# Kernel tuning notes

Hardware: AMD Instinct MI355X
Metric: run time of the kernel (lower is better)

## Reference

```python
import jax, jax.numpy as jnp
import numpy as np

B, T, D = 2, 2048, 2048
NH, NKV = 16, 4
HD = D // NH  # 128
BASE, TSL = 10000.0, 1024


def rotary_tables(T, hd, base=BASE, tsl=TSL):
    # Matches Rotary.forward with rd == hd (rd=0 in __init__ -> full head dim).
    ar = jnp.arange(0, hd, 2, dtype=jnp.float32) / hd
    if T <= tsl:
        inv = 1.0 / (base ** ar)
    else:
        # NTK-style rescale; note right-assoc exponent in original torch code:
        # 1/(base * (T/tsl) ** ((rd/(rd-2)) ** ar))
        inv = 1.0 / (base * jnp.power(T / tsl, jnp.power(hd / (hd - 2.0), ar)))
    f = jnp.outer(jnp.arange(T, dtype=jnp.float32), inv)  # [T, hd//2]
    cos = jnp.cos(f)[None, :, None, :]  # [1,T,1,hd//2]
    sin = jnp.sin(f)[None, :, None, :]
    return cos, sin


def apply_rope(x, cos, sin):
    # full-dim rope: split halves, rotate
    h = x.shape[-1] // 2
    x1, x2 = x[..., :h], x[..., h:]
    return jnp.concatenate((x1 * cos + x2 * sin, -x1 * sin + x2 * cos), axis=-1)


def rms_norm(x):
    eps = jnp.finfo(x.dtype).eps
    return x * jax.lax.rsqrt(jnp.mean(x * x, axis=-1, keepdims=True) + eps)


def setup_inputs() -> dict:
    key = jax.random.key(0)
    k0, k1, k2, k3, k4 = jax.random.split(key, 5)
    s = 0.02
    return {
        "x": jax.random.normal(k0, (B, T, D), jnp.float32),
        "qw": jax.random.normal(k1, (NH * HD, D), jnp.float32) * s,
        "kw": jax.random.normal(k2, (NKV * HD, D), jnp.float32) * s,
        "vw": jax.random.normal(k3, (NKV * HD, D), jnp.float32) * s,
        "ow": jax.random.normal(k4, (D, D), jnp.float32) * s,
        "qg": jnp.ones((NH,), jnp.float32),
    }


def reference(x, qw, kw, vw, ow, qg):
    Bx, Tx, Dx = x.shape
    q = (x @ qw.T).reshape(Bx, Tx, NH, HD)
    k = (x @ kw.T).reshape(Bx, Tx, NKV, HD)
    v = (x @ vw.T).reshape(Bx, Tx, NKV, HD)
    q = rms_norm(q)
    k = rms_norm(k)
    cos, sin = rotary_tables(Tx, HD)
    q = apply_rope(q, cos, sin) * qg[None, None, :, None]
    k = apply_rope(k, cos, sin)
    # GQA: repeat kv heads
    r = NH // NKV
    k = jnp.repeat(k, r, axis=2)  # [B,T,NH,HD]
    v = jnp.repeat(v, r, axis=2)
    scale = 1.0 / jnp.sqrt(jnp.asarray(HD, q.dtype))
    scores = jnp.einsum("bqhd,bkhd->bhqk", q, k) * scale  # [B,NH,T,T]
    causal = jnp.tril(jnp.ones((Tx, Tx), dtype=bool))
    scores = jnp.where(causal[None, None, :, :], scores, jnp.asarray(-jnp.inf, scores.dtype))
    attn = jax.nn.softmax(scores, axis=-1)
    y = jnp.einsum("bhqk,bkhd->bqhd", attn, v)  # [B,T,NH,HD]
    return y.reshape(Bx, Tx, Dx) @ ow.T
```

## Files before the change

kernel.cpp:

```cpp
#include <hip/hip_runtime.h>
#include <hip/hip_bf16.h>
#include <stdint.h>


typedef __attribute__((ext_vector_type(8))) short short8;
typedef __attribute__((ext_vector_type(4))) float f32x4;

#define GLOAD16(gp, lp) \
  __builtin_amdgcn_global_load_lds((const __attribute__((address_space(1))) void*)(gp), \
                                   (__attribute__((address_space(3))) void*)(lp), 16, 0, 0)

#define BAR() do { asm volatile("" ::: "memory"); __builtin_amdgcn_s_barrier(); asm volatile("" ::: "memory"); } while (0)

__device__ __forceinline__ float bf2f(unsigned short u) {
  union { unsigned int i; float f; } v; v.i = ((unsigned int)u) << 16; return v.f;
}
__device__ __forceinline__ unsigned short f2bf(float f) {
  union { float fl; unsigned int i; } v; v.fl = f;
  unsigned int r = v.i + 0x7fffu + ((v.i >> 16) & 1u);
  return (unsigned short)(r >> 16);
}

__global__ __launch_bounds__(256) void prep_kernel(
    const float* __restrict__ x, const float* __restrict__ qw,
    const float* __restrict__ kw, const float* __restrict__ vw,
    const float* __restrict__ ow,
    unsigned short* __restrict__ xb, unsigned short* __restrict__ wqkv,
    unsigned short* __restrict__ owb, float* __restrict__ cost, float* __restrict__ sint) {
  const int NX = 2097152;
  const int NW = 1572864;
  const int NO = 1048576;
  const int NT = 131072;
  int tid = blockIdx.x * 256 + threadIdx.x;
  if (tid < NX) {
    float4 v = ((const float4*)x)[tid];
    uint2 o; o.x = (unsigned)f2bf(v.x) | ((unsigned)f2bf(v.y) << 16);
    o.y = (unsigned)f2bf(v.z) | ((unsigned)f2bf(v.w) << 16);
    ((uint2*)xb)[tid] = o;
  } else if (tid < NX + NW) {
    int i = tid - NX; int e = i * 4;
    const float* src = (e < 4194304) ? (qw + e)
                     : (e < 5242880) ? (kw + (e - 4194304))
                                     : (vw + (e - 5242880));
    float4 v = *(const float4*)src;
    uint2 o; o.x = (unsigned)f2bf(v.x) | ((unsigned)f2bf(v.y) << 16);
    o.y = (unsigned)f2bf(v.z) | ((unsigned)f2bf(v.w) << 16);
    ((uint2*)wqkv)[i] = o;
  } else if (tid < NX + NW + NO) {
    int i = tid - NX - NW;
    float4 v = ((const float4*)ow)[i];
    uint2 o; o.x = (unsigned)f2bf(v.x) | ((unsigned)f2bf(v.y) << 16);
    o.y = (unsigned)f2bf(v.z) | ((unsigned)f2bf(v.w) << 16);
    ((uint2*)owb)[i] = o;
  } else if (tid < NX + NW + NO + NT) {
    int i = tid - NX - NW - NO;
    int t = i >> 6, j = i & 63;
    float e = exp2f(0.02272008f * (float)j * (1.0f / 64.0f));
    float inv = 1.0f / (10000.0f * exp2f(e));
    float f = (float)t * inv;
    cost[i] = cosf(f);
    sint[i] = sinf(f);
  }
}

template <int IM, int OUTF>
__global__ __launch_bounds__(512) void gemm8ph(const unsigned short* __restrict__ A,
                                               const unsigned short* __restrict__ Bw,
                                               void* __restrict__ Cp,
                                               int MT, int NTn, int N, int K) {
  extern __shared__ char smc[];
  constexpr int S = IM * 8;
  constexpr int IQ = IM / 2;
  constexpr int ASZ = IM * 2048;
  constexpr int DB = 2 * ASZ + 32768;
  constexpr int AL = (IM * 128) / 512;
  const int tid = threadIdx.x;
  const int l = tid & 63, w = tid >> 6;
  const int lane_r = l & 15, lane_g = l >> 4;
  const int wr = w >> 2, wc = w & 3;

  int qch = (MT * NTn) >> 3;
  int orig = blockIdx.x;
  int wgid = (orig & 7) * qch + (orig >> 3);
  int by = wgid / NTn, bx = wgid - by * NTn;
  const int m0 = by * IM * 32, n0 = bx * 256;

  f32x4 acc[IM][4];
#pragma unroll
  for (int i = 0; i < IM; ++i)
#pragma unroll
    for (int j = 0; j < 4; ++j) acc[i][j] = {0.f, 0.f, 0.f, 0.f};

  const unsigned short* srcA[AL]; int ldA[AL];
#pragma unroll
  for (int t = 0; t < AL; ++t) {
    int idx = t * 512 + tid;
    int rc = idx >> 3, kc = idx & 7;
    int wrp = rc >= S ? 1 : 0, rr = rc & (S - 1);
    int row = wrp * 2 * S + rr;
    srcA[t] = A + (size_t)(m0 + row) * K + (kc ^ (rc & 7)) * 8;
    ldA[t] = idx * 16;
  }
  const unsigned short* srcB[2]; int ldB[2];
#pragma unroll
  for (int t = 0; t < 2; ++t) {
    int idx = t * 512 + tid;
    int rc = idx >> 3, kc = idx & 7;
    int nrow = (rc >> 5) * 64 + (rc & 31);
    srcB[t] = Bw + (size_t)(n0 + nrow) * K + (kc ^ (rc & 7)) * 8;
    ldB[t] = idx * 16;
  }
  const int SK = S * K, JK = 32 * K;

  auto STA = [&](int kt, int ih, int dqb) {
    char* d = smc + dqb + ih * ASZ;
#pragma unroll
    for (int t = 0; t < AL; ++t) GLOAD16(srcA[t] + kt + ih * SK, d + ldA[t]);
  };
  auto STB = [&](int kt, int jh, int dqb) {
    char* d = smc + dqb + 2 * ASZ + jh * 16384;
#pragma unroll
    for (int t = 0; t < 2; ++t) GLOAD16(srcB[t] + kt + jh * JK, d + ldB[t]);
  };

  int oA[IQ][2], oB[2][2];
#pragma unroll
  for (int iq = 0; iq < IQ; ++iq)
#pragma unroll
    for (int ks = 0; ks < 2; ++ks) {
      int rc = wr * S + iq * 16 + lane_r;
      oA[iq][ks] = rc * 128 + ((ks * 64 + lane_g * 16) ^ ((rc & 7) << 4));
    }
#pragma unroll
  for (int jj = 0; jj < 2; ++jj)
#pragma unroll
    for (int ks = 0; ks < 2; ++ks) {
      int rc = wc * 32 + jj * 16 + lane_r;
      oB[jj][ks] = rc * 128 + ((ks * 64 + lane_g * 16) ^ ((rc & 7) << 4));
    }

#define VMC() do { if constexpr (IM == 8) asm volatile("s_waitcnt vmcnt(6)" ::: "memory"); \
                   else                   asm volatile("s_waitcnt vmcnt(5)" ::: "memory"); } while (0)
#define VM0() asm volatile("s_waitcnt vmcnt(0)" ::: "memory")
#define MM(IH, JH, BR) do { \
    __builtin_amdgcn_s_setprio(1); \
    _Pragma("unroll") \
    for (int iq = 0; iq < IQ; ++iq) \
      _Pragma("unroll") \
      for (int jj = 0; jj < 2; ++jj) \
        _Pragma("unroll") \
        for (int ks = 0; ks < 2; ++ks) \
          acc[(IH) * IQ + iq][(JH) * 2 + jj] = __builtin_amdgcn_mfma_f32_16x16x32_bf16( \
              af[iq][ks], BR[jj][ks], acc[(IH) * IQ + iq][(JH) * 2 + jj], 0, 0, 0); \
    __builtin_amdgcn_s_setprio(0); } while (0)

  const int NS = K >> 6;
  STA(0, 0, 0); STB(0, 0, 0); STB(0, 1, 0); STA(0, 1, 0);
  STA(64, 0, DB); STB(64, 0, DB); STB(64, 1, DB);
  VMC();
  BAR();

#pragma unroll 1
  for (int s = 0; s < NS; ++s) {
    const int dq = (s & 1) * DB, dn = DB - dq;
    const char* Ab = smc + dq;
    const char* Bb = Ab + 2 * ASZ;
    short8 af[IQ][2], b0[2][2], b1[2][2];
    if (s + 1 < NS) STA((s + 1) << 6, 1, dn);
#pragma unroll
    for (int iq = 0; iq < IQ; ++iq)
#pragma unroll
      for (int ks = 0; ks < 2; ++ks) af[iq][ks] = *(const short8*)(Ab + oA[iq][ks]);
#pragma unroll
    for (int jj = 0; jj < 2; ++jj)
#pragma unroll
      for (int ks = 0; ks < 2; ++ks) b0[jj][ks] = *(const short8*)(Bb + oB[jj][ks]);
    MM(0, 0, b0);
    BAR();
    if (s + 2 < NS) STA((s + 2) << 6, 0, dq);
#pragma unroll
    for (int jj = 0; jj < 2; ++jj)
#pragma unroll
      for (int ks = 0; ks < 2; ++ks) b1[jj][ks] = *(const short8*)(Bb + 16384 + oB[jj][ks]);
    MM(0, 1, b1);
    BAR();
    if (s + 2 < NS) STB((s + 2) << 6, 0, dq);
#pragma unroll
    for (int iq = 0; iq < IQ; ++iq)
#pragma unroll
      for (int ks = 0; ks < 2; ++ks) af[iq][ks] = *(const short8*)(Ab + ASZ + oA[iq][ks]);
    MM(1, 0, b0);
    BAR();
    if (s + 2 < NS) STB((s + 2) << 6, 1, dq);
    MM(1, 1, b1);
    if (s + 2 < NS) VMC(); else VM0();
    BAR();
  }
#undef VMC
#undef VM0
#undef MM

#pragma unroll
  for (int ih = 0; ih < 2; ++ih)
#pragma unroll
    for (int iq = 0; iq < IQ; ++iq) {
      int row = m0 + wr * 2 * S + ih * S + iq * 16 + lane_g * 4;
#pragma unroll
      for (int j = 0; j < 4; ++j) {
        int col = n0 + wc * 64 + j * 16 + lane_r;
#pragma unroll
        for (int r = 0; r < 4; ++r) {
          float v = acc[ih * IQ + iq][j][r];
          if (OUTF)
            ((float*)Cp)[(size_t)(row + r) * N + col] = v;
          else
            ((unsigned short*)Cp)[(size_t)(row + r) * N + col] = f2bf(v);
        }
      }
    }
}

__global__ __launch_bounds__(256) void normrope_kernel(unsigned short* __restrict__ qkv,
                                                       const float* __restrict__ cost,
                                                       const float* __restrict__ sint,
                                                       const float* __restrict__ qg) {
  const int tid = threadIdx.x, l = tid & 63, w = tid >> 6;
  int row = blockIdx.x * 4 + w;
  int tok = row / 20, hh = row - tok * 20;
  int t = tok & 2047;
  bool isq = hh < 16;
  int col0 = isq ? hh * 128 : 2048 + (hh - 16) * 128;
  unsigned short* p = qkv + (size_t)tok * 3072 + col0 + 2 * l;
  unsigned int u = *(const unsigned int*)p;
  float x0 = bf2f((unsigned short)(u & 0xffffu));
  float x1 = bf2f((unsigned short)(u >> 16));
  float ss = x0 * x0 + x1 * x1;
#pragma unroll
  for (int m = 1; m < 64; m <<= 1) ss += __shfl_xor(ss, m);
  float rn = rsqrtf(ss * (1.0f / 128.0f) + 1.1920928955078125e-07f);
  float n0 = x0 * rn, n1 = x1 * rn;
  float p0 = __shfl_xor(n0, 32);
  float p1 = __shfl_xor(n1, 32);
  int jj = (2 * l) & 63;
  float c0 = cost[t * 64 + jj], c1 = cost[t * 64 + jj + 1];
  float s0 = sint[t * 64 + jj], s1 = sint[t * 64 + jj + 1];
  float o0, o1;
  if (l < 32) { o0 = n0 * c0 + p0 * s0; o1 = n1 * c1 + p1 * s1; }
  else        { o0 = -p0 * s0 + n0 * c0; o1 = -p1 * s1 + n1 * c1; }
  if (isq) { float g = qg[hh] * 0.08838834764831845f; o0 *= g; o1 *= g; }
  *(unsigned int*)p = (unsigned)f2bf(o0) | ((unsigned)f2bf(o1) << 16);
}

__global__ __launch_bounds__(256) void vtrans_kernel(const unsigned short* __restrict__ qkv,
                                                     unsigned short* __restrict__ vtg) {
  __shared__ unsigned short tile[64][132];
  int bid = blockIdx.x;
  int pan = bid & 7, tt = bid >> 3;
  int b = pan >> 2, kvh = pan & 3;
  int t0 = tt * 64;
  const unsigned short* src = qkv + ((size_t)(b * 2048 + t0)) * 3072 + 2560 + kvh * 128;
#pragma unroll
  for (int i = 0; i < 8; ++i) {
    int idx = i * 256 + threadIdx.x;
    int row = idx >> 5, c4 = idx & 31;
    uint2 v = *(const uint2*)(src + (size_t)row * 3072 + c4 * 4);
    *(uint2*)&tile[row][c4 * 4] = v;
  }
  __syncthreads();
  unsigned short* dst = vtg + (size_t)pan * 262144 + t0;
#pragma unroll
  for (int i = 0; i < 8; ++i) {
    int idx = i * 256 + threadIdx.x;
    int d = idx >> 4, tc = idx & 15;
    unsigned short a0 = tile[tc * 4 + 0][d], a1 = tile[tc * 4 + 1][d];
    unsigned short a2 = tile[tc * 4 + 2][d], a3 = tile[tc * 4 + 3][d];
    uint2 o; o.x = (unsigned)a0 | ((unsigned)a1 << 16);
    o.y = (unsigned)a2 | ((unsigned)a3 << 16);
    *(uint2*)(dst + (size_t)d * 2048 + tc * 4) = o;
  }
}

__global__ __launch_bounds__(512) void attn_fa4(const unsigned short* __restrict__ qkv,
                                                const unsigned short* __restrict__ vtg,
                                                unsigned short* __restrict__ y) {
  extern __shared__ char smc[];
  const int tid = threadIdx.x;
  const int l = tid & 63, w = tid >> 6;
  const int lane_r = l & 15, lane_g = l >> 4;

  int n = blockIdx.x;
  int pan = n & 7;
  int b = pan >> 2, kvh = pan & 3;
  int idx2 = n >> 3;
  int h = kvh * 4 + (idx2 & 3);
  int pairIdx = idx2 >> 2;
  const size_t rowbase = (size_t)b * 2048;
  const unsigned short* kvK = qkv + rowbase * 3072;
  const unsigned short* vtp = vtg + (size_t)pan * 262144;

  int kg[2], vg[2], sl[2];
#pragma unroll
  for (int t = 0; t < 2; ++t) {
    int idx = t * 512 + tid;
    { int row = idx >> 4, c = idx & 15, gc = c ^ (row & 7);
      kg[t] = row * 3072 + 2048 + kvh * 128 + gc * 8; }
    { int d = idx >> 3, c = idx & 7, gc = c ^ (d & 7);
      vg[t] = d * 2048 + gc * 8; }
    sl[t] = idx * 16;
  }
  const int swz = (lane_r & 7) << 4;
  int oK[4][4];
#pragma unroll
  for (int ct = 0; ct < 4; ++ct)
#pragma unroll
    for (int ks = 0; ks < 4; ++ks)
      oK[ct][ks] = ((ct * 16 + lane_r) * 256 + ks * 64 + lane_g * 16) ^ swz;
  int oV[2][8];
#pragma unroll
  for (int kk = 0; kk < 2; ++kk)
#pragma unroll
    for (int dt = 0; dt < 8; ++dt)
      oV[kk][dt] = ((dt * 16 + lane_r) * 128 + kk * 64 + lane_g * 16) ^ swz;
  const int pbase = 65536 + w * 2048;
  int pw_off[4];
#pragma unroll
  for (int ct = 0; ct < 4; ++ct)
    pw_off[ct] = pbase + lane_r * 128 + ((ct * 32 + lane_g * 8) ^ swz);
  int pr_off[2];
#pragma unroll
  for (int kk = 0; kk < 2; ++kk)
    pr_off[kk] = pbase + lane_r * 128 + ((kk * 64 + lane_g * 16) ^ swz);

  auto STAGE = [&](int tile, int bufsel) {
    const unsigned short* srcK = kvK + (size_t)tile * 64 * 3072;
    const unsigned short* srcV = vtp + tile * 64;
    char* kd = smc + bufsel * 16384;
    char* vd = smc + 32768 + bufsel * 16384;
#pragma unroll
    for (int t = 0; t < 2; ++t) {
      GLOAD16(srcK + kg[t], kd + sl[t]);
      GLOAD16(srcV + vg[t], vd + sl[t]);
    }
  };

#pragma unroll 1
  for (int phase = 0; phase < 2; ++phase) {
    const int qt = phase ? pairIdx : 15 - pairIdx;
    const int q0 = qt * 128;
    const int nkb = 2 * qt + 2;
    const int wrow0 = q0 + w * 16;
    const int qrow = wrow0 + lane_r;

    STAGE(0, 0);
    short8 qf[4];
#pragma unroll
    for (int ks = 0; ks < 4; ++ks)
      qf[ks] = *(const short8*)(qkv + (rowbase + qrow) * 3072 + h * 128 + ks * 32 + lane_g * 8);

    f32x4 acc[8];
#pragma unroll
    for (int dt = 0; dt < 8; ++dt) acc[dt] = {0.f, 0.f, 0.f, 0.f};
    float mrun = -1e30f, lrun = 0.f;

    __syncthreads();

#pragma unroll 1
    for (int kb = 0; kb < nkb; ++kb) {
      const int cur = kb & 1;
      if (kb + 1 < nkb) STAGE(kb + 1, cur ^ 1);
      const int j0 = kb * 64;
      const bool active = (j0 <= wrow0 + 15);
      if (active) {
        const int kbb = cur * 16384;
        f32x4 s[4];
#pragma unroll
        for (int ct = 0; ct < 4; ++ct) s[ct] = {0.f, 0.f, 0.f, 0.f};
        __builtin_amdgcn_s_setprio(1);
#pragma unroll
        for (int ct = 0; ct < 4; ++ct)
#pragma unroll
          for (int ks = 0; ks < 4; ++ks) {
            short8 kf = *(const short8*)(smc + kbb + oK[ct][ks]);
            s[ct] = __builtin_amdgcn_mfma_f32_16x16x32_bf16(kf, qf[ks], s[ct], 0, 0, 0);
          }
        __builtin_amdgcn_s_setprio(0);
        if (j0 + 63 > wrow0) {
#pragma unroll
          for (int ct = 0; ct < 4; ++ct) {
            int kg0 = j0 + ct * 16 + lane_g * 4;
#pragma unroll
            for (int r = 0; r < 4; ++r)
              if (kg0 + r > qrow) s[ct][r] = -1e30f;
          }
        }
        float mx = s[0][0];
#pragma unroll
        for (int ct = 0; ct < 4; ++ct)
#pragma unroll
          for (int r = 0; r < 4; ++r) mx = fmaxf(mx, s[ct][r]);
        mx = fmaxf(mx, __shfl_xor(mx, 16));
        mx = fmaxf(mx, __shfl_xor(mx, 32));
        float mn = fmaxf(mrun, mx);
        float corr = __expf(mrun - mn);
        mrun = mn;
        float rs = 0.f;
#pragma unroll
        for (int ct = 0; ct < 4; ++ct)
#pragma unroll
          for (int r = 0; r < 4; ++r) {
            float e = __expf(s[ct][r] - mn);
            s[ct][r] = e; rs += e;
          }
        rs += __shfl_xor(rs, 16);
        rs += __shfl_xor(rs, 32);
        lrun = lrun * corr + rs;
#pragma unroll
        for (int ct = 0; ct < 4; ++ct) {
          uint2 pv;
          pv.x = (unsigned)f2bf(s[ct][0]) | ((unsigned)f2bf(s[ct][1]) << 16);
          pv.y = (unsigned)f2bf(s[ct][2]) | ((unsigned)f2bf(s[ct][3]) << 16);
          *(uint2*)(smc + pw_off[ct]) = pv;
        }
#pragma unroll
        for (int dt = 0; dt < 8; ++dt)
#pragma unroll
          for (int r = 0; r < 4; ++r) acc[dt][r] *= corr;
        short8 pf[2];
        pf[0] = *(const short8*)(smc + pr_off[0]);
        pf[1] = *(const short8*)(smc + pr_off[1]);
        const int vbase = 32768 + cur * 16384;
        __builtin_amdgcn_s_setprio(1);
#pragma unroll
        for (int kk = 0; kk < 2; ++kk)
#pragma unroll
          for (int dt = 0; dt < 8; ++dt) {
            short8 vf = *(const short8*)(smc + vbase + oV[kk][dt]);
            acc[dt] = __builtin_amdgcn_mfma_f32_16x16x32_bf16(vf, pf[kk], acc[dt], 0, 0, 0);
          }
        __builtin_amdgcn_s_setprio(0);
      }
      __syncthreads();
    }
    float linv = 1.0f / lrun;
    unsigned short* yrow = y + (rowbase + qrow) * 2048 + h * 128;
#pragma unroll
    for (int dt = 0; dt < 8; ++dt) {
      uint2 o;
      o.x = (unsigned)f2bf(acc[dt][0] * linv) | ((unsigned)f2bf(acc[dt][1] * linv) << 16);
      o.y = (unsigned)f2bf(acc[dt][2] * linv) | ((unsigned)f2bf(acc[dt][3] * linv) << 16);
      *(uint2*)(yrow + dt * 16 + lane_g * 4) = o;
    }
  }
}

extern "C" void kernel_launch(void* const* d_in, const int* in_sizes, int n_in,
                              void* d_out, int out_size, void* d_ws, size_t ws_size,
                              hipStream_t stream) {
  (void)in_sizes; (void)n_in; (void)out_size; (void)ws_size;
  const float* x  = (const float*)d_in[0];
  const float* qw = (const float*)d_in[1];
  const float* kw = (const float*)d_in[2];
  const float* vw = (const float*)d_in[3];
  const float* ow = (const float*)d_in[4];
  const float* qg = (const float*)d_in[5];

  char* ws = (char*)d_ws;
  unsigned short* xb   = (unsigned short*)(ws + 0);
  unsigned short* vtg  = (unsigned short*)(ws + 0);
  unsigned short* wqkv = (unsigned short*)(ws + 16777216);
  unsigned short* owb  = (unsigned short*)(ws + 29360128);
  unsigned short* qkvb = (unsigned short*)(ws + 37748736);
  unsigned short* y    = (unsigned short*)(ws + 62914560);
  float* cost          = (float*)(ws + 79691776);
  float* sint          = (float*)(ws + 80216064);

  prep_kernel<<<18944, 256, 0, stream>>>(x, qw, kw, vw, ow, xb, wqkv, owb, cost, sint);
  gemm8ph<8, 0><<<192, 512, 131072, stream>>>(xb, wqkv, qkvb, 16, 12, 3072, 2048);
  normrope_kernel<<<20480, 256, 0, stream>>>(qkvb, cost, sint, qg);
  vtrans_kernel<<<256, 256, 0, stream>>>(qkvb, vtg);
  attn_fa4<<<256, 512, 81920, stream>>>(qkvb, vtg, y);
  gemm8ph<4, 1><<<256, 512, 98304, stream>>>(y, owb, d_out, 32, 8, 2048, 2048);
}
```

Baseline: 200.4 us.

## Rewrite attention with 32x32 MFMA tiles, exp2 softmax and lazy rescaling

The attention kernel now runs 4 waves of 32 query rows each and uses 32x32x16 bf16 MFMAs instead of 16x16x32, which cuts LDS fragment loads and shuffle reductions per score tile. The log2(e) factor is folded into the q scale during norm/rope, so the softmax can use exp2 directly. Rescaling of the running max and accumulator is skipped unless the new max exceeds the old by more than a threshold. Each thread now carries larger accumulators, which raises register pressure, and the skipped rescale lets unnormalised values grow within a bounded range.

```diff
diff --git a/kernel.cpp b/kernel.cpp
--- a/kernel.cpp
+++ b/kernel.cpp
@@ -5,6 +5,7 @@
 
 typedef __attribute__((ext_vector_type(8))) short short8;
 typedef __attribute__((ext_vector_type(4))) float f32x4;
+typedef __attribute__((ext_vector_type(16))) float f32x16;
 
 #define GLOAD16(gp, lp) \
   __builtin_amdgcn_global_load_lds((const __attribute__((address_space(1))) void*)(gp), \
@@ -19,6 +20,9 @@
   union { float fl; unsigned int i; } v; v.fl = f;
   unsigned int r = v.i + 0x7fffu + ((v.i >> 16) & 1u);
   return (unsigned short)(r >> 16);
+}
+__device__ __forceinline__ unsigned pk2(float a, float b) {
+  return (unsigned)f2bf(a) | ((unsigned)f2bf(b) << 16);
 }
 
 __global__ __launch_bounds__(256) void prep_kernel(
@@ -34,8 +38,7 @@
   int tid = blockIdx.x * 256 + threadIdx.x;
   if (tid < NX) {
     float4 v = ((const float4*)x)[tid];
-    uint2 o; o.x = (unsigned)f2bf(v.x) | ((unsigned)f2bf(v.y) << 16);
-    o.y = (unsigned)f2bf(v.z) | ((unsigned)f2bf(v.w) << 16);
+    uint2 o; o.x = pk2(v.x, v.y); o.y = pk2(v.z, v.w);
     ((uint2*)xb)[tid] = o;
   } else if (tid < NX + NW) {
     int i = tid - NX; int e = i * 4;
@@ -43,14 +46,12 @@
                      : (e < 5242880) ? (kw + (e - 4194304))
                                      : (vw + (e - 5242880));
     float4 v = *(const float4*)src;
-    uint2 o; o.x = (unsigned)f2bf(v.x) | ((unsigned)f2bf(v.y) << 16);
-    o.y = (unsigned)f2bf(v.z) | ((unsigned)f2bf(v.w) << 16);
+    uint2 o; o.x = pk2(v.x, v.y); o.y = pk2(v.z, v.w);
     ((uint2*)wqkv)[i] = o;
   } else if (tid < NX + NW + NO) {
     int i = tid - NX - NW;
     float4 v = ((const float4*)ow)[i];
-    uint2 o; o.x = (unsigned)f2bf(v.x) | ((unsigned)f2bf(v.y) << 16);
-    o.y = (unsigned)f2bf(v.z) | ((unsigned)f2bf(v.w) << 16);
+    uint2 o; o.x = pk2(v.x, v.y); o.y = pk2(v.z, v.w);
     ((uint2*)owb)[i] = o;
   } else if (tid < NX + NW + NO + NT) {
     int i = tid - NX - NW - NO;
@@ -247,8 +248,8 @@
   float o0, o1;
   if (l < 32) { o0 = n0 * c0 + p0 * s0; o1 = n1 * c1 + p1 * s1; }
   else        { o0 = -p0 * s0 + n0 * c0; o1 = -p1 * s1 + n1 * c1; }
-  if (isq) { float g = qg[hh] * 0.08838834764831845f; o0 *= g; o1 *= g; }
-  *(unsigned int*)p = (unsigned)f2bf(o0) | ((unsigned)f2bf(o1) << 16);
+  if (isq) { float g = qg[hh] * 0.08838834764831845f * 1.4426950408889634f; o0 *= g; o1 *= g; }
+  *(unsigned int*)p = pk2(o0, o1);
 }
 
 __global__ __launch_bounds__(256) void vtrans_kernel(const unsigned short* __restrict__ qkv,
@@ -280,13 +281,13 @@
   }
 }
 
-__global__ __launch_bounds__(512) void attn_fa4(const unsigned short* __restrict__ qkv,
-                                                const unsigned short* __restrict__ vtg,
-                                                unsigned short* __restrict__ y) {
+__global__ __launch_bounds__(256, 2) void attn_fa5(const unsigned short* __restrict__ qkv,
+                                                   const unsigned short* __restrict__ vtg,
+                                                   unsigned short* __restrict__ y) {
   extern __shared__ char smc[];
   const int tid = threadIdx.x;
   const int l = tid & 63, w = tid >> 6;
-  const int lane_r = l & 15, lane_g = l >> 4;
+  const int lq = l & 31, hi = l >> 5;
 
   int n = blockIdx.x;
   int pan = n & 7;
@@ -298,38 +299,29 @@
   const unsigned short* kvK = qkv + rowbase * 3072;
   const unsigned short* vtp = vtg + (size_t)pan * 262144;
 
-  int kg[2], vg[2], sl[2];
-#pragma unroll
-  for (int t = 0; t < 2; ++t) {
-    int idx = t * 512 + tid;
+  int kg[4], vg[4], sl[4];
+#pragma unroll
+  for (int t = 0; t < 4; ++t) {
+    int idx = t * 256 + tid;
     { int row = idx >> 4, c = idx & 15, gc = c ^ (row & 7);
       kg[t] = row * 3072 + 2048 + kvh * 128 + gc * 8; }
     { int d = idx >> 3, c = idx & 7, gc = c ^ (d & 7);
       vg[t] = d * 2048 + gc * 8; }
     sl[t] = idx * 16;
   }
-  const int swz = (lane_r & 7) << 4;
-  int oK[4][4];
-#pragma unroll
-  for (int ct = 0; ct < 4; ++ct)
-#pragma unroll
-    for (int ks = 0; ks < 4; ++ks)
-      oK[ct][ks] = ((ct * 16 + lane_r) * 256 + ks * 64 + lane_g * 16) ^ swz;
-  int oV[2][8];
-#pragma unroll
-  for (int kk = 0; kk < 2; ++kk)
-#pragma unroll
-    for (int dt = 0; dt < 8; ++dt)
-      oV[kk][dt] = ((dt * 16 + lane_r) * 128 + kk * 64 + lane_g * 16) ^ swz;
-  const int pbase = 65536 + w * 2048;
-  int pw_off[4];
-#pragma unroll
-  for (int ct = 0; ct < 4; ++ct)
-    pw_off[ct] = pbase + lane_r * 128 + ((ct * 32 + lane_g * 8) ^ swz);
-  int pr_off[2];
-#pragma unroll
-  for (int kk = 0; kk < 2; ++kk)
-    pr_off[kk] = pbase + lane_r * 128 + ((kk * 64 + lane_g * 16) ^ swz);
+  const int swq = (lq & 7) << 4;
+  int oxd[8];
+#pragma unroll
+  for (int ds = 0; ds < 8; ++ds) oxd[ds] = (ds * 32 + hi * 16) ^ swq;
+  const int krow = lq * 256;
+  const int vrow = lq * 128;
+  const int pbase = 65536 + w * 4096;
+  const int prow = pbase + lq * 128;
+  int opw[2][4];
+#pragma unroll
+  for (int t = 0; t < 2; ++t)
+#pragma unroll
+    for (int m = 0; m < 4; ++m) opw[t][m] = prow + ((t * 64 + m * 16 + hi * 8) ^ swq);
 
   auto STAGE = [&](int tile, int bufsel) {
     const unsigned short* srcK = kvK + (size_t)tile * 64 * 3072;
@@ -337,7 +329,7 @@
     char* kd = smc + bufsel * 16384;
     char* vd = smc + 32768 + bufsel * 16384;
 #pragma unroll
-    for (int t = 0; t < 2; ++t) {
+    for (int t = 0; t < 4; ++t) {
       GLOAD16(srcK + kg[t], kd + sl[t]);
       GLOAD16(srcV + vg[t], vd + sl[t]);
     }
@@ -348,18 +340,20 @@
     const int qt = phase ? pairIdx : 15 - pairIdx;
     const int q0 = qt * 128;
     const int nkb = 2 * qt + 2;
-    const int wrow0 = q0 + w * 16;
-    const int qrow = wrow0 + lane_r;
+    const int wrow0 = q0 + w * 32;
+    const int qrow = wrow0 + lq;
 
     STAGE(0, 0);
-    short8 qf[4];
-#pragma unroll
-    for (int ks = 0; ks < 4; ++ks)
-      qf[ks] = *(const short8*)(qkv + (rowbase + qrow) * 3072 + h * 128 + ks * 32 + lane_g * 8);
-
-    f32x4 acc[8];
-#pragma unroll
-    for (int dt = 0; dt < 8; ++dt) acc[dt] = {0.f, 0.f, 0.f, 0.f};
+    short8 qf[8];
+#pragma unroll
+    for (int ds = 0; ds < 8; ++ds)
+      qf[ds] = *(const short8*)(qkv + (rowbase + qrow) * 3072 + h * 128 + ds * 16 + hi * 8);
+
+    f32x16 acc[4];
+#pragma unroll
+    for (int dt = 0; dt < 4; ++dt)
+#pragma unroll
+      for (int jj = 0; jj < 16; ++jj) acc[dt][jj] = 0.f;
     float mrun = -1e30f, lrun = 0.f;
 
     __syncthreads();
@@ -369,73 +363,74 @@
       const int cur = kb & 1;
       if (kb + 1 < nkb) STAGE(kb + 1, cur ^ 1);
       const int j0 = kb * 64;
-      const bool active = (j0 <= wrow0 + 15);
-      if (active) {
+      if (j0 <= wrow0 + 31) {
         const int kbb = cur * 16384;
-        f32x4 s[4];
-#pragma unroll
-        for (int ct = 0; ct < 4; ++ct) s[ct] = {0.f, 0.f, 0.f, 0.f};
+        const int vbb = 32768 + cur * 16384;
+        f32x16 s0, s1;
+#pragma unroll
+        for (int jj = 0; jj < 16; ++jj) { s0[jj] = 0.f; s1[jj] = 0.f; }
         __builtin_amdgcn_s_setprio(1);
 #pragma unroll
-        for (int ct = 0; ct < 4; ++ct)
-#pragma unroll
-          for (int ks = 0; ks < 4; ++ks) {
-            short8 kf = *(const short8*)(smc + kbb + oK[ct][ks]);
-            s[ct] = __builtin_amdgcn_mfma_f32_16x16x32_bf16(kf, qf[ks], s[ct], 0, 0, 0);
+        for (int ds = 0; ds < 8; ++ds) {
+          short8 kf = *(const short8*)(smc + kbb + krow + oxd[ds]);
+          s0 = __builtin_amdgcn_mfma_f32_32x32x16_bf16(kf, qf[ds], s0, 0, 0, 0);
+        }
+#pragma unroll
+        for (int ds = 0; ds < 8; ++ds) {
+          short8 kf = *(const short8*)(smc + kbb + 8192 + krow + oxd[ds]);
+          s1 = __builtin_amdgcn_mfma_f32_32x32x16_bf16(kf, qf[ds], s1, 0, 0, 0);
+        }
+        __builtin_amdgcn_s_setprio(0);
+        const int rq = qrow - j0;
+        if (j0 + 63 > wrow0) {
+#pragma unroll
+          for (int jj = 0; jj < 16; ++jj) {
+            int kl = (jj & 3) + 8 * (jj >> 2) + 4 * hi;
+            s0[jj] = (kl > rq) ? -1e30f : s0[jj];
+            s1[jj] = (kl + 32 > rq) ? -1e30f : s1[jj];
           }
-        __builtin_amdgcn_s_setprio(0);
-        if (j0 + 63 > wrow0) {
-#pragma unroll
-          for (int ct = 0; ct < 4; ++ct) {
-            int kg0 = j0 + ct * 16 + lane_g * 4;
-#pragma unroll
-            for (int r = 0; r < 4; ++r)
-              if (kg0 + r > qrow) s[ct][r] = -1e30f;
-          }
-        }
-        float mx = s[0][0];
-#pragma unroll
-        for (int ct = 0; ct < 4; ++ct)
-#pragma unroll
-          for (int r = 0; r < 4; ++r) mx = fmaxf(mx, s[ct][r]);
-        mx = fmaxf(mx, __shfl_xor(mx, 16));
-        mx = fmaxf(mx, __shfl_xor(mx, 32));
-        float mn = fmaxf(mrun, mx);
-        float corr = __expf(mrun - mn);
-        mrun = mn;
+        }
+        float pmax = s0[0];
+#pragma unroll
+        for (int jj = 0; jj < 16; ++jj) pmax = fmaxf(pmax, fmaxf(s0[jj], s1[jj]));
+        pmax = fmaxf(pmax, __shfl_xor(pmax, 32));
+        if (!__all(pmax - mrun <= 11.5f)) {
+          float mn = fmaxf(mrun, pmax);
+          float corr = exp2f(mrun - mn);
+          lrun *= corr;
+#pragma unroll
+          for (int dt = 0; dt < 4; ++dt)
+#pragma unroll
+            for (int jj = 0; jj < 16; ++jj) acc[dt][jj] *= corr;
+          mrun = mn;
+        }
         float rs = 0.f;
 #pragma unroll
-        for (int ct = 0; ct < 4; ++ct)
-#pragma unroll
-          for (int r = 0; r < 4; ++r) {
-            float e = __expf(s[ct][r] - mn);
-            s[ct][r] = e; rs += e;
-          }
-        rs += __shfl_xor(rs, 16);
+        for (int jj = 0; jj < 16; ++jj) {
+          s0[jj] = exp2f(s0[jj] - mrun); rs += s0[jj];
+          s1[jj] = exp2f(s1[jj] - mrun); rs += s1[jj];
+        }
         rs += __shfl_xor(rs, 32);
-        lrun = lrun * corr + rs;
-#pragma unroll
-        for (int ct = 0; ct < 4; ++ct) {
-          uint2 pv;
-          pv.x = (unsigned)f2bf(s[ct][0]) | ((unsigned)f2bf(s[ct][1]) << 16);
-          pv.y = (unsigned)f2bf(s[ct][2]) | ((unsigned)f2bf(s[ct][3]) << 16);
-          *(uint2*)(smc + pw_off[ct]) = pv;
-        }
-#pragma unroll
-        for (int dt = 0; dt < 8; ++dt)
-#pragma unroll
-          for (int r = 0; r < 4; ++r) acc[dt][r] *= corr;
-        short8 pf[2];
-        pf[0] = *(const short8*)(smc + pr_off[0]);
-        pf[1] = *(const short8*)(smc + pr_off[1]);
-        const int vbase = 32768 + cur * 16384;
+        lrun += rs;
+#pragma unroll
+        for (int m = 0; m < 4; ++m) {
+          uint2 p0, p1;
+          p0.x = pk2(s0[4 * m], s0[4 * m + 1]); p0.y = pk2(s0[4 * m + 2], s0[4 * m + 3]);
+          p1.x = pk2(s1[4 * m], s1[4 * m + 1]); p1.y = pk2(s1[4 * m + 2], s1[4 * m + 3]);
+          *(uint2*)(smc + opw[0][m]) = p0;
+          *(uint2*)(smc + opw[1][m]) = p1;
+        }
+        short8 pfr[4];
+#pragma unroll
+        for (int ksl = 0; ksl < 4; ++ksl)
+          pfr[ksl] = *(const short8*)(smc + prow + oxd[ksl]);
         __builtin_amdgcn_s_setprio(1);
 #pragma unroll
-        for (int kk = 0; kk < 2; ++kk)
-#pragma unroll
-          for (int dt = 0; dt < 8; ++dt) {
-            short8 vf = *(const short8*)(smc + vbase + oV[kk][dt]);
-            acc[dt] = __builtin_amdgcn_mfma_f32_16x16x32_bf16(vf, pf[kk], acc[dt], 0, 0, 0);
+        for (int ksl = 0; ksl < 4; ++ksl)
+#pragma unroll
+          for (int dt = 0; dt < 4; ++dt) {
+            short8 vf = *(const short8*)(smc + vbb + dt * 4096 + vrow + oxd[ksl]);
+            acc[dt] = __builtin_amdgcn_mfma_f32_32x32x16_bf16(vf, pfr[ksl], acc[dt], 0, 0, 0);
           }
         __builtin_amdgcn_s_setprio(0);
       }
@@ -444,12 +439,14 @@
     float linv = 1.0f / lrun;
     unsigned short* yrow = y + (rowbase + qrow) * 2048 + h * 128;
 #pragma unroll
-    for (int dt = 0; dt < 8; ++dt) {
-      uint2 o;
-      o.x = (unsigned)f2bf(acc[dt][0] * linv) | ((unsigned)f2bf(acc[dt][1] * linv) << 16);
-      o.y = (unsigned)f2bf(acc[dt][2] * linv) | ((unsigned)f2bf(acc[dt][3] * linv) << 16);
-      *(uint2*)(yrow + dt * 16 + lane_g * 4) = o;
-    }
+    for (int dt = 0; dt < 4; ++dt)
+#pragma unroll
+      for (int m = 0; m < 4; ++m) {
+        uint2 o;
+        o.x = pk2(acc[dt][4 * m] * linv, acc[dt][4 * m + 1] * linv);
+        o.y = pk2(acc[dt][4 * m + 2] * linv, acc[dt][4 * m + 3] * linv);
+        *(uint2*)(yrow + dt * 32 + m * 8 + hi * 4) = o;
+      }
   }
 }
 
@@ -478,6 +475,6 @@
   gemm8ph<8, 0><<<192, 512, 131072, stream>>>(xb, wqkv, qkvb, 16, 12, 3072, 2048);
   normrope_kernel<<<20480, 256, 0, stream>>>(qkvb, cost, sint, qg);
   vtrans_kernel<<<256, 256, 0, stream>>>(qkvb, vtg);
-  attn_fa4<<<256, 512, 81920, stream>>>(qkvb, vtg, y);
+  attn_fa5<<<256, 256, 81920, stream>>>(qkvb, vtg, y);
   gemm8ph<4, 1><<<256, 512, 98304, stream>>>(y, owb, d_out, 32, 8, 2048, 2048);
 }
```

Measured after the change: 214.6 us. 7.1% more time.
